# Kernel optimization log

Measured on AMD Instinct MI355X. Metric: run time of the kernel, lower is better.

The kernel has to match this reference:

```python
import jax, jax.numpy as jnp
import numpy as np

K_MAX = 64      # config.k_max
N_HASH = 8      # LSH hash bits per table


def setup_inputs() -> dict:
    key = jax.random.key(0)
    kq, kk, kw = jax.random.split(key, 3)
    B, L, D = 4, 2048, 64
    query = jax.random.normal(kq, (B, L, D), dtype=jnp.float32)
    key_t = jax.random.normal(kk, (B, L, D), dtype=jnp.float32)
    W = jax.random.normal(kw, (D, N_HASH), dtype=jnp.float32)  # LSH projection
    return {"query": query, "key": key_t, "W": W, "head_idx": 0}


def _hash_code(x, W):
    # binary_quantize then LSH hash: sign bits of random projection, packed to one int code
    x_bin = jnp.where(x > 0, 1.0, 0.0)                      # [B,L,D]
    bits = (jnp.einsum('bld,dh->blh', x_bin, W) > 0)        # [B,L,H] bool
    weights = (2 ** jnp.arange(N_HASH, dtype=jnp.int32))    # pack bits -> bucket id
    return jnp.sum(bits.astype(jnp.int32) * weights, axis=-1)  # [B,L] int32


def reference(query, key, W, head_idx):
    B, L, _ = query.shape
    q_code = _hash_code(query, W)   # [B,L]
    k_code = _hash_code(key, W)     # [B,L]
    # hash-equality match matrix [B, Lq, Lk] (== .all(dim=2) on hash bits)
    matches = q_code[:, :, None] == k_code[:, None, :]
    idx = jnp.arange(L, dtype=jnp.int32)
    # non-matches get sentinel L so the k_max smallest indices are the first matches
    cand_keys = jnp.where(matches, idx[None, None, :], L)   # [B,L,L]
    neg_top, _ = jax.lax.top_k(-cand_keys, K_MAX)           # k_max smallest indices
    cand = -neg_top                                          # ascending first-match order
    return jnp.where(cand == L, -1, cand).astype(jnp.int64)  # [B,L,k_max], -1 padded
```

## Files before the change

kernel.cpp:

```cpp
#include <hip/hip_runtime.h>

#define D 64
#define H 8
#define LSEQ 2048
#define KMAX 64
#define NCODES 256

__global__ void __launch_bounds__(64)
code_kernel(const float* __restrict__ query,
            const float* __restrict__ key,
            const float* __restrict__ W,
            int* __restrict__ q_code,
            unsigned char* __restrict__ kperm,
            int n_pos) {
    __shared__ float Ws[D * H];
    for (int i = threadIdx.x; i < D * H; i += blockDim.x) Ws[i] = W[i];
    __syncthreads();

    int t = blockIdx.x * blockDim.x + threadIdx.x;
    if (t >= 2 * n_pos) return;

    const float* xp = (t < n_pos) ? (query + (size_t)t * D)
                                  : (key + (size_t)(t - n_pos) * D);
    float4 s0 = {0.f, 0.f, 0.f, 0.f};
    float4 s1 = {0.f, 0.f, 0.f, 0.f};

    for (int d4 = 0; d4 < D / 4; ++d4) {
        float4 xv = ((const float4*)xp)[d4];
        const float* x4 = (const float*)&xv;
#pragma unroll
        for (int k = 0; k < 4; ++k) {
            if (x4[k] > 0.0f) {
                int d = d4 * 4 + k;
                float4 w0 = *(const float4*)&Ws[d * H + 0];
                float4 w1 = *(const float4*)&Ws[d * H + 4];
                s0.x += w0.x; s0.y += w0.y; s0.z += w0.z; s0.w += w0.w;
                s1.x += w1.x; s1.y += w1.y; s1.z += w1.z; s1.w += w1.w;
            }
        }
    }
    int c = 0;
    c |= (s0.x > 0.0f) ? 1   : 0;
    c |= (s0.y > 0.0f) ? 2   : 0;
    c |= (s0.z > 0.0f) ? 4   : 0;
    c |= (s0.w > 0.0f) ? 8   : 0;
    c |= (s1.x > 0.0f) ? 16  : 0;
    c |= (s1.y > 0.0f) ? 32  : 0;
    c |= (s1.z > 0.0f) ? 64  : 0;
    c |= (s1.w > 0.0f) ? 128 : 0;

    if (t < n_pos) {
        q_code[t] = c;
    } else {
        int kk = t - n_pos;
        int b    = kk >> 11;
        int l    = kk & (LSEQ - 1);
        int lane = l & 63;
        int j    = (l >> 6) & 3;
        int i4   = l >> 8;
        kperm[(b << 11) + (i4 << 8) + (lane << 2) + j] = (unsigned char)c;
    }
}

__global__ void __launch_bounds__(256)
scan_emit_kernel(const int* __restrict__ q_code,
                 const unsigned int* __restrict__ kperm,
                 int* __restrict__ out) {
    __shared__ int rows[4][KMAX];
    int wave = threadIdx.x >> 6;
    int lane = threadIdx.x & 63;
    int q = blockIdx.x * 4 + wave;
    int b = q >> 11;

    int c = q_code[q];
    const unsigned int* kp = kperm + (size_t)b * (LSEQ / 4) + lane;
    int* row = rows[wave];
    row[lane] = -1;

    unsigned int v[LSEQ / 256];
#pragma unroll
    for (int i = 0; i < LSEQ / 256; ++i) v[i] = kp[i * 64];

    unsigned long long lt_mask = (lane == 63) ? 0x7FFFFFFFFFFFFFFFull
                                              : ((1ull << lane) - 1ull);
    int base = 0;
#pragma unroll
    for (int i = 0; i < LSEQ / 256; ++i) {
        unsigned int w = v[i];
#pragma unroll
        for (int j = 0; j < 4; ++j) {
            int ci = (int)((w >> (8 * j)) & 0xFFu);
            unsigned long long mask = __ballot(ci == c);
            if (ci == c) {
                int rank = base + __popcll(mask & lt_mask);
                if (rank < KMAX) row[rank] = i * 256 + j * 64 + lane;
            }
            base += __popcll(mask);
        }
    }
    out[(size_t)q * KMAX + lane] = row[lane];
}

extern "C" void kernel_launch(void* const* d_in, const int* in_sizes, int n_in,
                              void* d_out, int out_size, void* d_ws, size_t ws_size,
                              hipStream_t stream) {
    const float* query = (const float*)d_in[0];
    const float* key   = (const float*)d_in[1];
    const float* W     = (const float*)d_in[2];

    int n_pos = in_sizes[0] / D;
    (void)ws_size;

    int* q_code = (int*)d_ws;
    unsigned char* kperm = (unsigned char*)(q_code + n_pos);

    {
        int total = 2 * n_pos;
        code_kernel<<<(total + 63) / 64, 64, 0, stream>>>(query, key, W,
                                                          q_code, kperm, n_pos);
    }
    {
        scan_emit_kernel<<<n_pos / 4, 256, 0, stream>>>(q_code,
                                                        (const unsigned int*)kperm,
                                                        (int*)d_out);
    }
}
```

Before: 73.87 us.

## Fuse hash-code and scan kernels into one cooperative kernel with grid sync

Merges the code computation and the match-scan into a single cooperative launch of 256 blocks, separated by a grid-wide barrier. Each wave now handles 8 queries and reuses its loaded key codes across them. This removes one kernel launch and the inter-kernel gap, but each wave's 8 queries run one after another and the grid sync adds its own cost. Sizes are now hardcoded through NPOS.

```diff
diff --git a/kernel.cpp b/kernel.cpp
--- a/kernel.cpp
+++ b/kernel.cpp
@@ -1,104 +1,111 @@
 #include <hip/hip_runtime.h>
+#include <hip/hip_cooperative_groups.h>
+
+namespace cg = cooperative_groups;
 
 #define D 64
 #define H 8
 #define LSEQ 2048
 #define KMAX 64
 #define NCODES 256
+#define NPOS 8192
 
-__global__ void __launch_bounds__(64)
-code_kernel(const float* __restrict__ query,
-            const float* __restrict__ key,
-            const float* __restrict__ W,
-            int* __restrict__ q_code,
-            unsigned char* __restrict__ kperm,
-            int n_pos) {
+__global__ void __launch_bounds__(256)
+fused_kernel(const float* __restrict__ query,
+             const float* __restrict__ key,
+             const float* __restrict__ W,
+             int* __restrict__ q_code,
+             unsigned char* __restrict__ kperm,
+             int* __restrict__ out) {
     __shared__ float Ws[D * H];
-    for (int i = threadIdx.x; i < D * H; i += blockDim.x) Ws[i] = W[i];
+    __shared__ int rows[4][KMAX];
+
+    int tid = threadIdx.x;
+    for (int i = tid; i < D * H; i += blockDim.x) Ws[i] = W[i];
     __syncthreads();
 
-    int t = blockIdx.x * blockDim.x + threadIdx.x;
-    if (t >= 2 * n_pos) return;
-
-    const float* xp = (t < n_pos) ? (query + (size_t)t * D)
-                                  : (key + (size_t)(t - n_pos) * D);
-    float4 s0 = {0.f, 0.f, 0.f, 0.f};
-    float4 s1 = {0.f, 0.f, 0.f, 0.f};
-
-    for (int d4 = 0; d4 < D / 4; ++d4) {
-        float4 xv = ((const float4*)xp)[d4];
-        const float* x4 = (const float*)&xv;
+    int t = blockIdx.x * blockDim.x + tid;
+    if (t < 2 * NPOS) {
+        const float* xp = (t < NPOS) ? (query + (size_t)t * D)
+                                     : (key + (size_t)(t - NPOS) * D);
+        float4 s0 = {0.f, 0.f, 0.f, 0.f};
+        float4 s1 = {0.f, 0.f, 0.f, 0.f};
+        for (int d4 = 0; d4 < D / 4; ++d4) {
+            float4 xv = ((const float4*)xp)[d4];
+            const float* x4 = (const float*)&xv;
 #pragma unroll
-        for (int k = 0; k < 4; ++k) {
-            if (x4[k] > 0.0f) {
-                int d = d4 * 4 + k;
-                float4 w0 = *(const float4*)&Ws[d * H + 0];
-                float4 w1 = *(const float4*)&Ws[d * H + 4];
-                s0.x += w0.x; s0.y += w0.y; s0.z += w0.z; s0.w += w0.w;
-                s1.x += w1.x; s1.y += w1.y; s1.z += w1.z; s1.w += w1.w;
+            for (int k = 0; k < 4; ++k) {
+                if (x4[k] > 0.0f) {
+                    int d = d4 * 4 + k;
+                    float4 w0 = *(const float4*)&Ws[d * H + 0];
+                    float4 w1 = *(const float4*)&Ws[d * H + 4];
+                    s0.x += w0.x; s0.y += w0.y; s0.z += w0.z; s0.w += w0.w;
+                    s1.x += w1.x; s1.y += w1.y; s1.z += w1.z; s1.w += w1.w;
+                }
             }
         }
+        int c = 0;
+        c |= (s0.x > 0.0f) ? 1   : 0;
+        c |= (s0.y > 0.0f) ? 2   : 0;
+        c |= (s0.z > 0.0f) ? 4   : 0;
+        c |= (s0.w > 0.0f) ? 8   : 0;
+        c |= (s1.x > 0.0f) ? 16  : 0;
+        c |= (s1.y > 0.0f) ? 32  : 0;
+        c |= (s1.z > 0.0f) ? 64  : 0;
+        c |= (s1.w > 0.0f) ? 128 : 0;
+
+        if (t < NPOS) {
+            q_code[t] = c;
+        } else {
+            int kk   = t - NPOS;
+            int b    = kk >> 11;
+            int l    = kk & (LSEQ - 1);
+            int lane = l & 63;
+            int j    = (l >> 6) & 3;
+            int i4   = l >> 8;
+            kperm[(b << 11) + (i4 << 8) + (lane << 2) + j] = (unsigned char)c;
+        }
     }
-    int c = 0;
-    c |= (s0.x > 0.0f) ? 1   : 0;
-    c |= (s0.y > 0.0f) ? 2   : 0;
-    c |= (s0.z > 0.0f) ? 4   : 0;
-    c |= (s0.w > 0.0f) ? 8   : 0;
-    c |= (s1.x > 0.0f) ? 16  : 0;
-    c |= (s1.y > 0.0f) ? 32  : 0;
-    c |= (s1.z > 0.0f) ? 64  : 0;
-    c |= (s1.w > 0.0f) ? 128 : 0;
 
-    if (t < n_pos) {
-        q_code[t] = c;
-    } else {
-        int kk = t - n_pos;
-        int b    = kk >> 11;
-        int l    = kk & (LSEQ - 1);
-        int lane = l & 63;
-        int j    = (l >> 6) & 3;
-        int i4   = l >> 8;
-        kperm[(b << 11) + (i4 << 8) + (lane << 2) + j] = (unsigned char)c;
-    }
-}
+    __threadfence();
+    cg::this_grid().sync();
+    __threadfence();
 
-__global__ void __launch_bounds__(256)
-scan_emit_kernel(const int* __restrict__ q_code,
-                 const unsigned int* __restrict__ kperm,
-                 int* __restrict__ out) {
-    __shared__ int rows[4][KMAX];
-    int wave = threadIdx.x >> 6;
-    int lane = threadIdx.x & 63;
-    int q = blockIdx.x * 4 + wave;
-    int b = q >> 11;
+    int wave = tid >> 6;
+    int lane = tid & 63;
+    int w = blockIdx.x * 4 + wave;
+    int q0 = w * 8;
+    int b = q0 >> 11;
 
-    int c = q_code[q];
-    const unsigned int* kp = kperm + (size_t)b * (LSEQ / 4) + lane;
-    int* row = rows[wave];
-    row[lane] = -1;
-
+    const unsigned int* kp = (const unsigned int*)kperm + (size_t)b * (LSEQ / 4) + lane;
     unsigned int v[LSEQ / 256];
 #pragma unroll
     for (int i = 0; i < LSEQ / 256; ++i) v[i] = kp[i * 64];
 
+    int* row = rows[wave];
     unsigned long long lt_mask = (lane == 63) ? 0x7FFFFFFFFFFFFFFFull
                                               : ((1ull << lane) - 1ull);
-    int base = 0;
+    for (int qq = 0; qq < 8; ++qq) {
+        int q = q0 + qq;
+        int c = q_code[q];
+        row[lane] = -1;
+        int base = 0;
 #pragma unroll
-    for (int i = 0; i < LSEQ / 256; ++i) {
-        unsigned int w = v[i];
+        for (int i = 0; i < LSEQ / 256; ++i) {
+            unsigned int w4 = v[i];
 #pragma unroll
-        for (int j = 0; j < 4; ++j) {
-            int ci = (int)((w >> (8 * j)) & 0xFFu);
-            unsigned long long mask = __ballot(ci == c);
-            if (ci == c) {
-                int rank = base + __popcll(mask & lt_mask);
-                if (rank < KMAX) row[rank] = i * 256 + j * 64 + lane;
+            for (int j = 0; j < 4; ++j) {
+                int ci = (int)((w4 >> (8 * j)) & 0xFFu);
+                unsigned long long mask = __ballot(ci == c);
+                if (ci == c) {
+                    int rank = base + __popcll(mask & lt_mask);
+                    if (rank < KMAX) row[rank] = i * 256 + j * 64 + lane;
+                }
+                base += __popcll(mask);
             }
-            base += __popcll(mask);
         }
+        out[(size_t)q * KMAX + lane] = row[lane];
     }
-    out[(size_t)q * KMAX + lane] = row[lane];
 }
 
 extern "C" void kernel_launch(void* const* d_in, const int* in_sizes, int n_in,
@@ -107,21 +114,14 @@
     const float* query = (const float*)d_in[0];
     const float* key   = (const float*)d_in[1];
     const float* W     = (const float*)d_in[2];
-
-    int n_pos = in_sizes[0] / D;
-    (void)ws_size;
+    (void)in_sizes; (void)n_in; (void)out_size; (void)ws_size;
 
     int* q_code = (int*)d_ws;
-    unsigned char* kperm = (unsigned char*)(q_code + n_pos);
+    unsigned char* kperm = (unsigned char*)(q_code + NPOS);
+    int* out = (int*)d_out;
 
-    {
-        int total = 2 * n_pos;
-        code_kernel<<<(total + 63) / 64, 64, 0, stream>>>(query, key, W,
-                                                          q_code, kperm, n_pos);
-    }
-    {
-        scan_emit_kernel<<<n_pos / 4, 256, 0, stream>>>(q_code,
-                                                        (const unsigned int*)kperm,
-                                                        (int*)d_out);
-    }
+    void* args[] = {(void*)&query, (void*)&key, (void*)&W,
+                    (void*)&q_code, (void*)&kperm, (void*)&out};
+    hipLaunchCooperativeKernel((const void*)fused_kernel,
+                               dim3(256), dim3(256), args, 0, stream);
 }
```

Result: slower. 147.4 us (+99.5%).
